# Kernel tuning notes

Hardware: AMD Instinct MI355X
Metric: run time of the kernel (lower is better)

The kernel has to match this reference:

```python
import jax, jax.numpy as jnp
import numpy as np

B, IN_DIM, N, L = 8, 2, 512, 64
D_MODEL = 32
D_FF = 32          # must equal D_MODEL: output_bn is BatchNorm2d(d_model) applied to skip
DEPTH = 3          # blocks=3 * layers=1; dilation resets to 1 each block -> all dilations = 1
KS = 2             # temporal kernel size
EPS = 1e-5         # BatchNorm eps


def setup_inputs() -> dict:
    key = jax.random.key(0)
    ks = jax.random.split(key, 16)
    s = 0.1  # weight scale for numeric sanity
    x = jax.random.normal(ks[0], (B, IN_DIM, N, L), jnp.float32)
    a = jax.random.uniform(ks[1], (N, N), jnp.float32)
    adj = a / a.sum(axis=1, keepdims=True)  # row-stochastic diffusion matrix
    return {
        "x": x,
        "adj": adj,
        "Wstart": jax.random.normal(ks[2], (D_MODEL, IN_DIM), jnp.float32) * s,
        "bstart": jnp.zeros((D_MODEL,), jnp.float32),
        "Wf": jax.random.normal(ks[3], (DEPTH, D_MODEL, D_MODEL, KS), jnp.float32) * s,
        "bf": jnp.zeros((DEPTH, D_MODEL), jnp.float32),
        "Wg": jax.random.normal(ks[4], (DEPTH, D_MODEL, D_MODEL, KS), jnp.float32) * s,
        "bg": jnp.zeros((DEPTH, D_MODEL), jnp.float32),
        "Wskip": jax.random.normal(ks[5], (DEPTH, D_FF, D_MODEL), jnp.float32) * s,
        "bskip": jnp.zeros((DEPTH, D_FF), jnp.float32),
        "Wgc": jax.random.normal(ks[6], (DEPTH, D_MODEL, 3 * D_MODEL), jnp.float32) * s,
        "bgc": jnp.zeros((DEPTH, D_MODEL), jnp.float32),
        "gcbn_g": jnp.ones((DEPTH, D_MODEL), jnp.float32),
        "gcbn_b": jnp.zeros((DEPTH, D_MODEL), jnp.float32),
        "bn_g": jnp.ones((DEPTH, D_MODEL), jnp.float32),
        "bn_b": jnp.zeros((DEPTH, D_MODEL), jnp.float32),
        "obn_g": jnp.ones((D_MODEL,), jnp.float32),
        "obn_b": jnp.zeros((D_MODEL,), jnp.float32),
    }


def _c1x1(x, W, b):
    # Conv2d with (1,1) kernel == channel mixing. x: [b,c,n,l], W: [o,c]
    return jnp.einsum('bcnl,oc->bonl', x, W) + b[None, :, None, None]


def _dconv(x, W, b, d):
    # Conv2d kernel (1,2), dilation d along time (valid). W: [o,c,2]
    Lx = x.shape[-1]
    y = (jnp.einsum('bcnl,oc->bonl', x[..., :Lx - d], W[..., 0])
         + jnp.einsum('bcnl,oc->bonl', x[..., d:], W[..., 1]))
    return y + b[None, :, None, None]


def _bn(x, g, bta):
    # eval-mode BatchNorm2d: running_mean=0, running_var=1
    inv = g / jnp.sqrt(1.0 + EPS)
    return x * inv[None, :, None, None] + bta[None, :, None, None]


def reference(x, adj, Wstart, bstart, Wf, bf, Wg, bg, Wskip, bskip,
              Wgc, bgc, gcbn_g, gcbn_b, bn_g, bn_b, obn_g, obn_b):
    rf = 1 + DEPTH * (KS - 1)  # receptive field with dilation 1 per layer
    h = _c1x1(x, Wstart, bstart)
    if h.shape[-1] < rf:
        h = jnp.pad(h, ((0, 0), (0, 0), (0, 0), (rf - h.shape[-1], 0)))
    skip = None
    for i in range(DEPTH):
        residual = h
        filt = jnp.tanh(_dconv(h, Wf[i], bf[i], 1))
        gate = jax.nn.sigmoid(_dconv(h, Wg[i], bg[i], 1))
        h = filt * gate
        s = _c1x1(h, Wskip[i], bskip[i])
        skip = s if skip is None else s + skip[..., -s.shape[-1]:]
        if i == DEPTH - 1:
            break
        # order-2 graph diffusion: h, A h, A^2 h -> concat -> 1x1 conv -> BN (dropout: eval noop)
        x1 = jnp.einsum('bcnl,nm->bcml', h, adj)
        x2 = jnp.einsum('bcnl,nm->bcml', x1, adj)
        cat = jnp.concatenate([h, x1, x2], axis=1)
        g = _bn(_c1x1(cat, Wgc[i], bgc[i]), gcbn_g[i], gcbn_b[i])
        h = g + residual[..., -g.shape[-1]:]
        h = _bn(h, bn_g[i], bn_b[i])
    out = _bn(skip, obn_g, obn_b)
    return jnp.swapaxes(out, 1, 3)  # [B, L', N, C]
```

## Files before the change

### kernel.cpp

```cpp
#include <hip/hip_runtime.h>
#include <hip/hip_bf16.h>

#define B_     8
#define CIN_   2
#define N_     512
#define C_     32
#define L_     64
#define LOUT_  61
#define BUF_   ((size_t)(8*32*512*64))

typedef __hip_bfloat16 bf16;
typedef unsigned short ushort_t;
typedef unsigned int u32;
typedef __attribute__((ext_vector_type(8))) unsigned short us8;
typedef __attribute__((ext_vector_type(8))) short bf16x8;
typedef __attribute__((ext_vector_type(4))) float f32x4;

static __device__ __forceinline__ float bits2f(ushort_t u) {
    return __uint_as_float(((unsigned)u) << 16);
}
static __device__ __forceinline__ ushort_t f2bits(float v) {
    unsigned u = __float_as_uint(v);
    return (ushort_t)((u + 0x7fffu + ((u >> 16) & 1u)) >> 16);
}

static __device__ __forceinline__ void gload16(const ushort_t* g, ushort_t* l) {
    __builtin_amdgcn_global_load_lds(
        (const __attribute__((address_space(1))) unsigned int*)g,
        (__attribute__((address_space(3))) unsigned int*)l,
        16, 0, 0);
}

static __device__ __forceinline__ u32 swap1(u32 v) {
    return (u32)__builtin_amdgcn_update_dpp(0, (int)v, 0xB1, 0xF, 0xF, true);
}

__global__ void k_start(const float* __restrict__ x,
                        const float* __restrict__ Wst,
                        const float* __restrict__ bst,
                        ushort_t* __restrict__ h) {
    int idx = blockIdx.x * 256 + threadIdx.x;
    int l0 = (idx & 7) * 8;
    int n  = (idx >> 3) & 511;
    int o  = (idx >> 12) & 31;
    int b  = idx >> 17;
    float w0 = Wst[o * 2], w1 = Wst[o * 2 + 1], bb = bst[o];
    int xbase = (b * CIN_ * N_ + n) * L_ + l0;
    float va[8], vb[8];
    *(float4*)&va[0] = *(const float4*)(x + xbase);
    *(float4*)&va[4] = *(const float4*)(x + xbase + 4);
    *(float4*)&vb[0] = *(const float4*)(x + xbase + N_ * L_);
    *(float4*)&vb[4] = *(const float4*)(x + xbase + N_ * L_ + 4);
    us8 r;
    #pragma unroll
    for (int k = 0; k < 8; ++k) r[k] = f2bits(bb + va[k] * w0 + vb[k] * w1);
    *(us8*)(h + (size_t)idx * 8) = r;
}

__global__ void k_transA(const float* __restrict__ adj, ushort_t* __restrict__ adjT) {
    __shared__ float buf[64][65];
    int ti = blockIdx.x & 7;
    int tj = blockIdx.x >> 3;
    int t = threadIdx.x;
    for (int r = 0; r < 16; ++r) {
        int e = t + 256 * r;
        int rl = e >> 6, cl = e & 63;
        buf[rl][cl] = adj[(size_t)(ti * 64 + rl) * 512 + tj * 64 + cl];
    }
    __syncthreads();
    for (int r = 0; r < 16; ++r) {
        int e = t + 256 * r;
        int ml = e >> 6, nl = e & 63;
        adjT[(size_t)(tj * 64 + ml) * 512 + ti * 64 + nl] = f2bits(buf[nl][ml]);
    }
}

__global__ __launch_bounds__(256, 2) void k_sq(const ushort_t* __restrict__ adjT,
                                               ushort_t* __restrict__ adj2T) {
    __shared__ __align__(16) ushort_t lds2[8192];
    ushort_t* As = lds2;
    ushort_t* Bs = lds2 + 4096;
    int mt = blockIdx.x & 7, nc = blockIdx.x >> 3;
    int t = threadIdx.x, lane = t & 63, w = t >> 6;
    int la = lane & 15, q = lane >> 4;
    f32x4 acc[4];
    #pragma unroll
    for (int mi = 0; mi < 4; ++mi) acc[mi] = (f32x4)0.f;
    for (int p0 = 0; p0 < 512; p0 += 64) {
        __syncthreads();
        #pragma unroll
        for (int r = 0; r < 2; ++r) {
            int e = t + 256 * r, ml = e >> 3, oct = e & 7;
            int sw = ((oct + (ml >> 3)) & 7) << 3;
            *(us8*)(As + ml * 64 + sw) =
                *(const us8*)(adjT + (size_t)(mt * 64 + ml) * 512 + p0 + oct * 8);
            *(us8*)(Bs + ml * 64 + sw) =
                *(const us8*)(adjT + (size_t)(p0 + ml) * 512 + nc * 64 + oct * 8);
        }
        __syncthreads();
        #pragma unroll
        for (int ks = 0; ks < 2; ++ks) {
            bf16x8 a[4];
            #pragma unroll
            for (int mi = 0; mi < 4; ++mi) {
                int m = mi * 16 + la;
                int bl = (ks * 4 + q + (m >> 3)) & 7;
                a[mi] = *(const bf16x8*)(As + m * 64 + bl * 8);
            }
            bf16x8 bv;
            {
                int n = w * 16 + la;
                int rot = ((n >> 3) + ks * 4 + q) & 7;
                int col = rot * 8 + (n & 7);
                const ushort_t* p = Bs + (ks * 32 + q * 8) * 64 + col;
                #pragma unroll
                for (int j = 0; j < 8; ++j) bv[j] = (short)p[j * 64];
            }
            #pragma unroll
            for (int mi = 0; mi < 4; ++mi)
                acc[mi] = __builtin_amdgcn_mfma_f32_16x16x32_bf16(a[mi], bv, acc[mi], 0, 0, 0);
        }
    }
    __syncthreads();
    ushort_t* Ys = lds2;
    #pragma unroll
    for (int mi = 0; mi < 4; ++mi)
        #pragma unroll
        for (int r = 0; r < 4; ++r)
            Ys[(mi * 16 + q * 4 + r) * 72 + w * 16 + la] = f2bits(acc[mi][r]);
    __syncthreads();
    #pragma unroll
    for (int r = 0; r < 2; ++r) {
        int e = t + 256 * r, ml = e >> 3, oct = e & 7;
        us8 v = *(const us8*)(Ys + ml * 72 + oct * 8);
        *(us8*)(adj2T + (size_t)(mt * 64 + ml) * 512 + nc * 64 + oct * 8) = v;
    }
}

__global__ __launch_bounds__(256, 4) void k_gs_mfma(
        const ushort_t* __restrict__ h,
        const float* __restrict__ Wf, const float* __restrict__ bfp,
        const float* __restrict__ Wg, const float* __restrict__ bgp,
        const float* __restrict__ Wsk, const float* __restrict__ bsk,
        ushort_t* __restrict__ G, float* __restrict__ out,
        int off, int mode, int storeG,
        const float* __restrict__ og, const float* __restrict__ obb) {
    __shared__ __align__(16) ushort_t lds[9984];
    ushort_t* Hs  = lds;
    ushort_t* Asf = lds + 4096;
    ushort_t* Asg = lds + 6400;
    ushort_t* As2 = lds + 8704;
    __shared__ float bfv[32], bgv[32], bsv[32];
    int t = threadIdx.x;
    int b = blockIdx.x >> 8, n0 = (blockIdx.x & 255) * 2;
    int lane = t & 63, w = t >> 6;
    int ng = w & 1, cg = w >> 1;
    int la = lane & 15, q = lane >> 4;

    const ushort_t* hb = h + (size_t)(b * 32) * 512 * 64;
    #pragma unroll
    for (int r = 0; r < 2; ++r) {
        int e = t + 256 * r;
        int row = e >> 3, s = e & 7;
        int og_ = ((s - row - (row >> 5)) & 7) * 8;
        gload16(hb + ((size_t)(row >> 1) * 512 + n0 + (row & 1)) * 64 + og_,
                Hs + (size_t)e * 8);
    }
    {
        int o = t >> 3, k8 = (t & 7) * 8;
        us8 vf, vg;
        #pragma unroll
        for (int i = 0; i < 8; ++i) {
            int k = k8 + i, c = k & 31, tap = k >> 5;
            vf[i] = f2bits(Wf[o * 64 + c * 2 + tap]);
            vg[i] = f2bits(Wg[o * 64 + c * 2 + tap]);
        }
        *(us8*)(Asf + o * 72 + k8) = vf;
        *(us8*)(Asg + o * 72 + k8) = vg;
        if (k8 < 32) {
            us8 vs;
            #pragma unroll
            for (int i = 0; i < 8; ++i) vs[i] = f2bits(Wsk[o * 32 + k8 + i]);
            *(us8*)(As2 + o * 40 + k8) = vs;
        }
        if (t < 32) { bfv[t] = bfp[t]; bgv[t] = bgp[t]; bsv[t] = bsk[t]; }
    }
    float4 oldv[4];
    #pragma unroll
    for (int i = 0; i < 4; ++i) oldv[i] = make_float4(0.f, 0.f, 0.f, 0.f);
    {
        int col = t >> 1, o0 = (t & 1) * 16;
        int nr = col >> 6, l = col & 63;
        if (mode != 0 && l < LOUT_) {
            const float* po = out + ((size_t)(b * LOUT_ + l) * 512 + n0 + nr) * 32 + o0;
            #pragma unroll
            for (int i = 0; i < 4; ++i) oldv[i] = *(const float4*)(po + i * 4);
        }
    }
    __syncthreads();

    bf16x8 af[2][2], ag[2][2];
    #pragma unroll
    for (int mt = 0; mt < 2; ++mt)
        #pragma unroll
        for (int ks = 0; ks < 2; ++ks) {
            af[mt][ks] = *(const bf16x8*)(Asf + (mt * 16 + la) * 72 + ks * 32 + q * 8);
            ag[mt][ks] = *(const bf16x8*)(Asg + (mt * 16 + la) * 72 + ks * 32 + q * 8);
        }
    bf16x8 a2[2];
    a2[0] = *(const bf16x8*)(As2 + la * 40 + q * 8);
    a2[1] = *(const bf16x8*)(As2 + (16 + la) * 40 + q * 8);

    f32x4 fa[2][2], ga[2][2];
    #pragma unroll
    for (int mt = 0; mt < 2; ++mt)
        #pragma unroll
        for (int cl = 0; cl < 2; ++cl) { fa[mt][cl] = (f32x4)0.f; ga[mt][cl] = (f32x4)0.f; }
    #pragma unroll
    for (int cl = 0; cl < 2; ++cl) {
        int ct = cg * 2 + cl;
        #pragma unroll
        for (int ks = 0; ks < 2; ++ks) {
            int le = ct * 16 + la + ks;
            bf16x8 bv;
            #pragma unroll
            for (int j = 0; j < 8; ++j) {
                int row = (q * 8 + j) * 2 + ng;
                int slot = ((le >> 3) + row + (row >> 5)) & 7;
                bv[j] = (le < 64) ? (short)Hs[row * 64 + (slot & 7) * 8 + (le & 7)] : (short)0;
            }
            #pragma unroll
            for (int mt = 0; mt < 2; ++mt) {
                fa[mt][cl] = __builtin_amdgcn_mfma_f32_16x16x32_bf16(af[mt][ks], bv, fa[mt][cl], 0, 0, 0);
                ga[mt][cl] = __builtin_amdgcn_mfma_f32_16x16x32_bf16(ag[mt][ks], bv, ga[mt][cl], 0, 0, 0);
            }
        }
    }
    __syncthreads();

    #pragma unroll
    for (int mt = 0; mt < 2; ++mt)
        #pragma unroll
        for (int cl = 0; cl < 2; ++cl)
            #pragma unroll
            for (int r = 0; r < 4; ++r) {
                int o = mt * 16 + q * 4 + r;
                float fv = fa[mt][cl][r] + bfv[o];
                float gv = ga[mt][cl][r] + bgv[o];
                float ef = __expf(2.f * fv);
                float act = (1.f - 2.f / (ef + 1.f)) * (1.f / (1.f + __expf(-gv)));
                int l = (cg * 2 + cl) * 16 + la;
                int row = o * 2 + ng;
                int slot = ((l >> 3) + row + (row >> 5)) & 7;
                Hs[row * 64 + slot * 8 + (l & 7)] = f2bits(act);
            }
    __syncthreads();

    if (storeG) {
        #pragma unroll
        for (int r = 0; r < 2; ++r) {
            int e = t + 256 * r;
            int row = e >> 3, s = e & 7;
            int og_ = (s - row - (row >> 5)) & 7;
            us8 v = *(const us8*)(Hs + (size_t)e * 8);
            *(us8*)(G + ((size_t)(b * 32 + (row >> 1)) * 512 + n0 + (row & 1)) * 64 + og_ * 8) = v;
        }
    }
    f32x4 sa[2][2];
    #pragma unroll
    for (int mt = 0; mt < 2; ++mt)
        #pragma unroll
        for (int cl = 0; cl < 2; ++cl) sa[mt][cl] = (f32x4)0.f;
    #pragma unroll
    for (int cl = 0; cl < 2; ++cl) {
        int le = (cg * 2 + cl) * 16 + la + off;
        bf16x8 bv;
        #pragma unroll
        for (int j = 0; j < 8; ++j) {
            int row = (q * 8 + j) * 2 + ng;
            int slot = ((le >> 3) + row + (row >> 5)) & 7;
            bv[j] = (le < 64) ? (short)Hs[row * 64 + (slot & 7) * 8 + (le & 7)] : (short)0;
        }
        sa[0][cl] = __builtin_amdgcn_mfma_f32_16x16x32_bf16(a2[0], bv, sa[0][cl], 0, 0, 0);
        sa[1][cl] = __builtin_amdgcn_mfma_f32_16x16x32_bf16(a2[1], bv, sa[1][cl], 0, 0, 0);
    }
    __syncthreads();

    float* St = (float*)lds;
    const float rbn = rsqrtf(1.f + 1e-5f);
    #pragma unroll
    for (int mt = 0; mt < 2; ++mt)
        #pragma unroll
        for (int cl = 0; cl < 2; ++cl) {
            int col = ng * 64 + (cg * 2 + cl) * 16 + la;
            int ob = mt * 16 + q * 4;
            float4 sv = make_float4(sa[mt][cl][0] + bsv[ob],
                                    sa[mt][cl][1] + bsv[ob + 1],
                                    sa[mt][cl][2] + bsv[ob + 2],
                                    sa[mt][cl][3] + bsv[ob + 3]);
            *(float4*)(St + col * 36 + ob) = sv;
        }
    __syncthreads();
    {
        int col = t >> 1, o0 = (t & 1) * 16;
        int nr = col >> 6, l = col & 63;
        if (l < LOUT_) {
            float* po = out + ((size_t)(b * LOUT_ + l) * 512 + n0 + nr) * 32 + o0;
            #pragma unroll
            for (int i = 0; i < 4; ++i) {
                float4 s = *(float4*)(St + col * 36 + o0 + i * 4);
                if (mode == 0) {
                    *(float4*)(po + i * 4) = s;
                } else {
                    float4 vv = make_float4(oldv[i].x + s.x, oldv[i].y + s.y,
                                            oldv[i].z + s.z, oldv[i].w + s.w);
                    if (mode == 2) {
                        int ob = o0 + i * 4;
                        vv.x = vv.x * (og[ob] * rbn) + obb[ob];
                        vv.y = vv.y * (og[ob + 1] * rbn) + obb[ob + 1];
                        vv.z = vv.z * (og[ob + 2] * rbn) + obb[ob + 2];
                        vv.w = vv.w * (og[ob + 3] * rbn) + obb[ob + 3];
                    }
                    *(float4*)(po + i * 4) = vv;
                }
            }
        }
    }
}

__global__ __launch_bounds__(256, 2) void k_diffuse2(
        const ushort_t* __restrict__ X, const ushort_t* __restrict__ adjT,
        const ushort_t* __restrict__ adj2T,
        ushort_t* __restrict__ Y1, ushort_t* __restrict__ Y2) {
    __shared__ __align__(16) ushort_t lds[32768];
    int cp = blockIdx.x & 15;
    int mt = (blockIdx.x >> 4) & 7;
    int b  = blockIdx.x >> 7;
    int t  = threadIdx.x;
    int lane = t & 63, w = t >> 6;
    int c_loc = w & 1, lh = w >> 1;
    int m0 = mt * 64;
    int la = lane & 15, q = lane >> 4;
    int p_ = la & 1;
    u32 sel = p_ ? 0x07060302u : 0x05040100u;
    const ushort_t* Xb = X + (size_t)(b * 32 + cp * 2) * 512 * 64;
    f32x4 acc1[4][2], acc2[4][2];
    #pragma unroll
    for (int mi = 0; mi < 4; ++mi)
        #pragma unroll
        for (int li = 0; li < 2; ++li) { acc1[mi][li] = (f32x4)0.f; acc2[mi][li] = (f32x4)0.f; }

    union U { u32 u[4]; bf16x8 v; };

    auto STAGE = [&](int n0, ushort_t* bb) {
        ushort_t* As1b = bb;
        ushort_t* As2b = bb + 4096;
        ushort_t* Xsb  = bb + 8192;
        #pragma unroll
        for (int r = 0; r < 2; ++r) {
            int e = t + 256 * r, ml = e >> 3, s = e & 7;
            int og = ((s - (ml >> 3)) & 7) * 8;
            gload16(adjT  + (size_t)(m0 + ml) * 512 + n0 + og, As1b + (size_t)e * 8);
            gload16(adj2T + (size_t)(m0 + ml) * 512 + n0 + og, As2b + (size_t)e * 8);
        }
        #pragma unroll
        for (int r = 0; r < 4; ++r) {
            int e = t + 256 * r;
            int cl = e >> 9, nl = (e >> 3) & 63, s = e & 7;
            int og = ((s - nl - (nl >> 3)) & 7) * 8;
            gload16(Xb + ((size_t)cl * 512 + n0 + nl) * 64 + og, Xsb + (size_t)e * 8);
        }
    };

    STAGE(0, lds);
    __syncthreads();

    for (int it = 0; it < 8; ++it) {
        ushort_t* cur = lds + (it & 1) * 16384;
        if (it < 7) STAGE((it + 1) * 64, lds + ((it + 1) & 1) * 16384);
        ushort_t* As1 = cur;
        ushort_t* As2 = cur + 4096;
        ushort_t* Xs  = cur + 8192;
        const ushort_t* xc = Xs + c_loc * 4096;
        #pragma unroll
        for (int ks = 0; ks < 2; ++ks) {
            bf16x8 a1[4], a2v[4];
            #pragma unroll
            for (int mi = 0; mi < 4; ++mi) {
                int m = mi * 16 + la;
                int bl = (ks * 4 + q + (m >> 3)) & 7;
                a1[mi]  = *(const bf16x8*)(As1 + m * 64 + bl * 8);
                a2v[mi] = *(const bf16x8*)(As2 + m * 64 + bl * 8);
            }
            bf16x8 bb[2];
            #pragma unroll
            for (int li = 0; li < 2; ++li) {
                int l2 = lh * 32 + li * 16 + (la & ~1);
                int r0 = ks * 32 + q * 8 + p_ * 4;
                int brot = ((l2 >> 3) + p_ * 4 + ks * 4 + q) & 7;
                u32 o0 = *(const u32*)(xc + (r0 + 0) * 64 + (((brot + 0) & 7) << 3) + (l2 & 7));
                u32 o1 = *(const u32*)(xc + (r0 + 1) * 64 + (((brot + 1) & 7) << 3) + (l2 & 7));
                u32 o2 = *(const u32*)(xc + (r0 + 2) * 64 + (((brot + 2) & 7) << 3) + (l2 & 7));
                u32 o3 = *(const u32*)(xc + (r0 + 3) * 64 + (((brot + 3) & 7) << 3) + (l2 & 7));
                u32 s0 = swap1(o0), s1 = swap1(o1), s2 = swap1(o2), s3 = swap1(o3);
                u32 lo0 = p_ ? s0 : o0, lo1 = p_ ? s1 : o1;
                u32 lo2 = p_ ? s2 : o2, lo3 = p_ ? s3 : o3;
                u32 hi0 = p_ ? o0 : s0, hi1 = p_ ? o1 : s1;
                u32 hi2 = p_ ? o2 : s2, hi3 = p_ ? o3 : s3;
                U u;
                u.u[0] = __builtin_amdgcn_perm(lo1, lo0, sel);
                u.u[1] = __builtin_amdgcn_perm(lo3, lo2, sel);
                u.u[2] = __builtin_amdgcn_perm(hi1, hi0, sel);
                u.u[3] = __builtin_amdgcn_perm(hi3, hi2, sel);
                bb[li] = u.v;
            }
            #pragma unroll
            for (int mi = 0; mi < 4; ++mi)
                #pragma unroll
                for (int li = 0; li < 2; ++li) {
                    acc1[mi][li] = __builtin_amdgcn_mfma_f32_16x16x32_bf16(a1[mi],  bb[li], acc1[mi][li], 0, 0, 0);
                    acc2[mi][li] = __builtin_amdgcn_mfma_f32_16x16x32_bf16(a2v[mi], bb[li], acc2[mi][li], 0, 0, 0);
                }
        }
        __syncthreads();
    }

    ushort_t* Ys = lds;
    #pragma unroll
    for (int pass = 0; pass < 2; ++pass) {
        __syncthreads();
        f32x4 (*src)[2] = pass ? acc2 : acc1;
        #pragma unroll
        for (int mi = 0; mi < 4; ++mi)
            #pragma unroll
            for (int li = 0; li < 2; ++li)
                #pragma unroll
                for (int r = 0; r < 4; ++r) {
                    int row = mi * 16 + q * 4 + r;
                    int col = lh * 32 + li * 16 + la;
                    Ys[c_loc * 4608 + row * 72 + col] = f2bits(src[mi][li][r]);
                }
        __syncthreads();
        ushort_t* Yo = pass ? Y2 : Y1;
        int c = t >> 7, mrem = t & 127;
        int m = mrem >> 1, lq = mrem & 1;
        #pragma unroll
        for (int r = 0; r < 4; ++r) {
            int l0 = lq * 32 + r * 8;
            us8 v = *(const us8*)(Ys + c * 4608 + m * 72 + l0);
            *(us8*)(Yo + ((size_t)(b * 32 + cp * 2 + c) * 512 + m0 + m) * 64 + l0) = v;
        }
    }
}

__global__ __launch_bounds__(256, 4) void k_gc3_mfma(
        ushort_t* __restrict__ G, const ushort_t* __restrict__ X1,
        const ushort_t* __restrict__ X2, const ushort_t* __restrict__ hres,
        const float* __restrict__ Wgc, const float* __restrict__ bgc,
        const float* __restrict__ gg, const float* __restrict__ gb,
        const float* __restrict__ bg2, const float* __restrict__ bb2) {
    __shared__ __align__(16) ushort_t cat[192 * 64];
    __shared__ __align__(16) ushort_t hr[64 * 64];
    __shared__ __align__(16) ushort_t Aw[32 * 104];
    __shared__ float prm[5][32];
    int t = threadIdx.x;
    int b = blockIdx.x >> 8, n0 = (blockIdx.x & 255) * 2;
    int lane = t & 63, w = t >> 6;
    int ng = w & 1, cg = w >> 1;
    int la = lane & 15, q = lane >> 4;
    int p_ = la & 1;
    u32 sel = p_ ? 0x07060302u : 0x05040100u;

    #pragma unroll
    for (int r = 0; r < 6; ++r) {
        int e = t + 256 * r;
        int row = e >> 3, s = e & 7;
        int k = row >> 1, nr = row & 1;
        int rot = k + (k >> 3);
        int og = ((s - rot) & 7) * 8;
        const ushort_t* src = (k < 32) ? G : ((k < 64) ? X1 : X2);
        gload16(src + ((size_t)(b * 32 + (k & 31)) * 512 + n0 + nr) * 64 + og,
                cat + (size_t)e * 8);
    }
    #pragma unroll
    for (int r = 0; r < 2; ++r) {
        int e = t + 256 * r;
        int row = e >> 3, oct = e & 7;
        gload16(hres + ((size_t)(b * 32 + (row >> 1)) * 512 + n0 + (row & 1)) * 64 + oct * 8,
                hr + (size_t)e * 8);
    }
    for (int e = t; e < 384; e += 256) {
        int o = e / 12, oct = e % 12;
        us8 v;
        #pragma unroll
        for (int i = 0; i < 8; ++i) v[i] = f2bits(Wgc[o * 96 + oct * 8 + i]);
        *(us8*)(Aw + o * 104 + oct * 8) = v;
    }
    if (t < 32) {
        prm[0][t] = bgc[t]; prm[1][t] = gg[t]; prm[2][t] = gb[t];
        prm[3][t] = bg2[t]; prm[4][t] = bb2[t];
    }
    __syncthreads();

    bf16x8 a[2][3];
    #pragma unroll
    for (int mt = 0; mt < 2; ++mt)
        #pragma unroll
        for (int ks = 0; ks < 3; ++ks)
            a[mt][ks] = *(const bf16x8*)(Aw + (mt * 16 + la) * 104 + ks * 32 + q * 8);

    union U { u32 u[4]; bf16x8 v; };
    f32x4 acc[2][2];
    #pragma unroll
    for (int mt = 0; mt < 2; ++mt)
        #pragma unroll
        for (int cl = 0; cl < 2; ++cl) acc[mt][cl] = (f32x4)0.f;
    #pragma unroll
    for (int cl = 0; cl < 2; ++cl) {
        int l2 = (cg * 2 + cl) * 16 + (la & ~1);
        #pragma unroll
        for (int ks = 0; ks < 3; ++ks) {
            int rb = (ks * 64 + q * 16 + p_ * 8 + ng);
            int brot = ((l2 >> 3) + p_ * 4 + ks * 4 + q) & 7;
            u32 o0 = *(const u32*)(cat + (rb + 0) * 64 + (((brot + 0) & 7) << 3) + (l2 & 7));
            u32 o1 = *(const u32*)(cat + (rb + 2) * 64 + (((brot + 1) & 7) << 3) + (l2 & 7));
            u32 o2 = *(const u32*)(cat + (rb + 4) * 64 + (((brot + 2) & 7) << 3) + (l2 & 7));
            u32 o3 = *(const u32*)(cat + (rb + 6) * 64 + (((brot + 3) & 7) << 3) + (l2 & 7));
            u32 s0 = swap1(o0), s1 = swap1(o1), s2 = swap1(o2), s3 = swap1(o3);
            u32 lo0 = p_ ? s0 : o0, lo1 = p_ ? s1 : o1;
            u32 lo2 = p_ ? s2 : o2, lo3 = p_ ? s3 : o3;
            u32 hi0 = p_ ? o0 : s0, hi1 = p_ ? o1 : s1;
            u32 hi2 = p_ ? o2 : s2, hi3 = p_ ? o3 : s3;
            U u;
            u.u[0] = __builtin_amdgcn_perm(lo1, lo0, sel);
            u.u[1] = __builtin_amdgcn_perm(lo3, lo2, sel);
            u.u[2] = __builtin_amdgcn_perm(hi1, hi0, sel);
            u.u[3] = __builtin_amdgcn_perm(hi3, hi2, sel);
            acc[0][cl] = __builtin_amdgcn_mfma_f32_16x16x32_bf16(a[0][ks], u.v, acc[0][cl], 0, 0, 0);
            acc[1][cl] = __builtin_amdgcn_mfma_f32_16x16x32_bf16(a[1][ks], u.v, acc[1][cl], 0, 0, 0);
        }
    }
    __syncthreads();

    const float rbn = rsqrtf(1.f + 1e-5f);
    #pragma unroll
    for (int mt = 0; mt < 2; ++mt)
        #pragma unroll
        for (int cl = 0; cl < 2; ++cl)
            #pragma unroll
            for (int r = 0; r < 4; ++r) {
                int o = mt * 16 + q * 4 + r;
                int l = (cg * 2 + cl) * 16 + la;
                float v = acc[mt][cl][r] + prm[0][o];
                v = v * (prm[1][o] * rbn) + prm[2][o];
                float res = (l < 63) ? bits2f(hr[(o * 2 + ng) * 64 + l + 1]) : 0.f;
                v = (v + res) * (prm[3][o] * rbn) + prm[4][o];
                int row = o * 2 + ng;
                int rot = o + (o >> 3);
                int slot = ((l >> 3) + rot) & 7;
                cat[row * 64 + slot * 8 + (l & 7)] = f2bits(v);
            }
    __syncthreads();
    #pragma unroll
    for (int r = 0; r < 2; ++r) {
        int e = t + 256 * r;
        int row = e >> 3, og = e & 7;
        int o = row >> 1, nr = row & 1;
        int slot = (og + o + (o >> 3)) & 7;
        us8 v = *(const us8*)(cat + row * 64 + slot * 8);
        *(us8*)(G + ((size_t)(b * 32 + o) * 512 + n0 + nr) * 64 + og * 8) = v;
    }
}

extern "C" void kernel_launch(void* const* d_in, const int* in_sizes, int n_in,
                              void* d_out, int out_size, void* d_ws, size_t ws_size,
                              hipStream_t stream) {
    const float* x      = (const float*)d_in[0];
    const float* adj    = (const float*)d_in[1];
    const float* Wstart = (const float*)d_in[2];
    const float* bstart = (const float*)d_in[3];
    const float* Wf     = (const float*)d_in[4];
    const float* bf_    = (const float*)d_in[5];
    const float* Wg     = (const float*)d_in[6];
    const float* bg     = (const float*)d_in[7];
    const float* Wskip  = (const float*)d_in[8];
    const float* bskip  = (const float*)d_in[9];
    const float* Wgc    = (const float*)d_in[10];
    const float* bgc    = (const float*)d_in[11];
    const float* gcbn_g = (const float*)d_in[12];
    const float* gcbn_b = (const float*)d_in[13];
    const float* bn_g   = (const float*)d_in[14];
    const float* bn_b   = (const float*)d_in[15];
    const float* obn_g  = (const float*)d_in[16];
    const float* obn_b  = (const float*)d_in[17];
    float* out = (float*)d_out;

    ushort_t* P0    = (ushort_t*)d_ws;
    ushort_t* P1    = P0 + BUF_;
    ushort_t* P2    = P1 + BUF_;
    ushort_t* P3    = P2 + BUF_;
    ushort_t* adjT  = P3 + BUF_;
    ushort_t* adj2T = adjT + 512 * 512;

    k_transA<<<64, 256, 0, stream>>>(adj, adjT);
    k_sq<<<64, 256, 0, stream>>>(adjT, adj2T);
    k_start<<<4096, 256, 0, stream>>>(x, Wstart, bstart, P0);

    ushort_t* h  = P0;
    ushort_t* Gb = P1;
    for (int i = 0; i < 3; ++i) {
        int mode = (i == 0) ? 0 : ((i == 2) ? 2 : 1);
        k_gs_mfma<<<2048, 256, 0, stream>>>(h, Wf + i * 2048, bf_ + i * 32,
                                            Wg + i * 2048, bg + i * 32,
                                            Wskip + i * 1024, bskip + i * 32,
                                            Gb, out, 2 - i, mode, (i < 2) ? 1 : 0,
                                            obn_g, obn_b);
        if (i == 2) break;
        k_diffuse2<<<1024, 256, 0, stream>>>(Gb, adjT, adj2T, P2, P3);
        k_gc3_mfma<<<2048, 256, 0, stream>>>(Gb, P2, P3, h,
                                             Wgc + i * 3072, bgc + i * 32,
                                             gcbn_g + i * 32, gcbn_b + i * 32,
                                             bn_g + i * 32, bn_b + i * 32);
        ushort_t* tmp = h; h = Gb; Gb = tmp;
    }
}
```

Before: 303.4 us.

## Retile diffusion kernel to one channel per block, load adjacency directly from global

The diffusion kernel now handles one channel per block instead of two, doubling the grid and halving LDS so four blocks fit per CU. Adjacency A and A^2 fragments are read straight from global memory into registers rather than staged through shared memory; only the X tile is double-buffered in LDS. The aim is higher occupancy and less LDS traffic. The cost is that each block re-reads the adjacency tiles from global/L2 with half the reuse per load, which adds cache pressure.

```diff
diff --git a/kernel.cpp b/kernel.cpp
--- a/kernel.cpp
+++ b/kernel.cpp
@@ -328,47 +328,34 @@
     }
 }
 
-__global__ __launch_bounds__(256, 2) void k_diffuse2(
+__global__ __launch_bounds__(256, 4) void k_diffuse2(
         const ushort_t* __restrict__ X, const ushort_t* __restrict__ adjT,
         const ushort_t* __restrict__ adj2T,
         ushort_t* __restrict__ Y1, ushort_t* __restrict__ Y2) {
-    __shared__ __align__(16) ushort_t lds[32768];
-    int cp = blockIdx.x & 15;
-    int mt = (blockIdx.x >> 4) & 7;
-    int b  = blockIdx.x >> 7;
+    __shared__ __align__(16) ushort_t lds[16384];
+    int c  = blockIdx.x & 31;
+    int mt = (blockIdx.x >> 5) & 7;
+    int b  = blockIdx.x >> 8;
     int t  = threadIdx.x;
     int lane = t & 63, w = t >> 6;
-    int c_loc = w & 1, lh = w >> 1;
     int m0 = mt * 64;
     int la = lane & 15, q = lane >> 4;
     int p_ = la & 1;
     u32 sel = p_ ? 0x07060302u : 0x05040100u;
-    const ushort_t* Xb = X + (size_t)(b * 32 + cp * 2) * 512 * 64;
-    f32x4 acc1[4][2], acc2[4][2];
-    #pragma unroll
-    for (int mi = 0; mi < 4; ++mi)
-        #pragma unroll
-        for (int li = 0; li < 2; ++li) { acc1[mi][li] = (f32x4)0.f; acc2[mi][li] = (f32x4)0.f; }
+    const ushort_t* Xb = X + (size_t)(b * 32 + c) * 512 * 64;
+    f32x4 acc1[4], acc2[4];
+    #pragma unroll
+    for (int mi = 0; mi < 4; ++mi) { acc1[mi] = (f32x4)0.f; acc2[mi] = (f32x4)0.f; }
 
     union U { u32 u[4]; bf16x8 v; };
 
-    auto STAGE = [&](int n0, ushort_t* bb) {
-        ushort_t* As1b = bb;
-        ushort_t* As2b = bb + 4096;
-        ushort_t* Xsb  = bb + 8192;
+    auto STAGE = [&](int n0, ushort_t* Xsb) {
         #pragma unroll
         for (int r = 0; r < 2; ++r) {
-            int e = t + 256 * r, ml = e >> 3, s = e & 7;
-            int og = ((s - (ml >> 3)) & 7) * 8;
-            gload16(adjT  + (size_t)(m0 + ml) * 512 + n0 + og, As1b + (size_t)e * 8);
-            gload16(adj2T + (size_t)(m0 + ml) * 512 + n0 + og, As2b + (size_t)e * 8);
-        }
-        #pragma unroll
-        for (int r = 0; r < 4; ++r) {
             int e = t + 256 * r;
-            int cl = e >> 9, nl = (e >> 3) & 63, s = e & 7;
+            int nl = e >> 3, s = e & 7;
             int og = ((s - nl - (nl >> 3)) & 7) * 8;
-            gload16(Xb + ((size_t)cl * 512 + n0 + nl) * 64 + og, Xsb + (size_t)e * 8);
+            gload16(Xb + ((size_t)(n0 + nl)) * 64 + og, Xsb + (size_t)e * 8);
         }
     };
 
@@ -376,51 +363,40 @@
     __syncthreads();
 
     for (int it = 0; it < 8; ++it) {
-        ushort_t* cur = lds + (it & 1) * 16384;
-        if (it < 7) STAGE((it + 1) * 64, lds + ((it + 1) & 1) * 16384);
-        ushort_t* As1 = cur;
-        ushort_t* As2 = cur + 4096;
-        ushort_t* Xs  = cur + 8192;
-        const ushort_t* xc = Xs + c_loc * 4096;
+        ushort_t* Xs = lds + (it & 1) * 8192;
+        if (it < 7) STAGE((it + 1) * 64, lds + ((it + 1) & 1) * 8192);
+        int n0 = it * 64;
         #pragma unroll
         for (int ks = 0; ks < 2; ++ks) {
             bf16x8 a1[4], a2v[4];
             #pragma unroll
             for (int mi = 0; mi < 4; ++mi) {
-                int m = mi * 16 + la;
-                int bl = (ks * 4 + q + (m >> 3)) & 7;
-                a1[mi]  = *(const bf16x8*)(As1 + m * 64 + bl * 8);
-                a2v[mi] = *(const bf16x8*)(As2 + m * 64 + bl * 8);
-            }
-            bf16x8 bb[2];
-            #pragma unroll
-            for (int li = 0; li < 2; ++li) {
-                int l2 = lh * 32 + li * 16 + (la & ~1);
-                int r0 = ks * 32 + q * 8 + p_ * 4;
-                int brot = ((l2 >> 3) + p_ * 4 + ks * 4 + q) & 7;
-                u32 o0 = *(const u32*)(xc + (r0 + 0) * 64 + (((brot + 0) & 7) << 3) + (l2 & 7));
-                u32 o1 = *(const u32*)(xc + (r0 + 1) * 64 + (((brot + 1) & 7) << 3) + (l2 & 7));
-                u32 o2 = *(const u32*)(xc + (r0 + 2) * 64 + (((brot + 2) & 7) << 3) + (l2 & 7));
-                u32 o3 = *(const u32*)(xc + (r0 + 3) * 64 + (((brot + 3) & 7) << 3) + (l2 & 7));
-                u32 s0 = swap1(o0), s1 = swap1(o1), s2 = swap1(o2), s3 = swap1(o3);
-                u32 lo0 = p_ ? s0 : o0, lo1 = p_ ? s1 : o1;
-                u32 lo2 = p_ ? s2 : o2, lo3 = p_ ? s3 : o3;
-                u32 hi0 = p_ ? o0 : s0, hi1 = p_ ? o1 : s1;
-                u32 hi2 = p_ ? o2 : s2, hi3 = p_ ? o3 : s3;
-                U u;
-                u.u[0] = __builtin_amdgcn_perm(lo1, lo0, sel);
-                u.u[1] = __builtin_amdgcn_perm(lo3, lo2, sel);
-                u.u[2] = __builtin_amdgcn_perm(hi1, hi0, sel);
-                u.u[3] = __builtin_amdgcn_perm(hi3, hi2, sel);
-                bb[li] = u.v;
-            }
-            #pragma unroll
-            for (int mi = 0; mi < 4; ++mi)
-                #pragma unroll
-                for (int li = 0; li < 2; ++li) {
-                    acc1[mi][li] = __builtin_amdgcn_mfma_f32_16x16x32_bf16(a1[mi],  bb[li], acc1[mi][li], 0, 0, 0);
-                    acc2[mi][li] = __builtin_amdgcn_mfma_f32_16x16x32_bf16(a2v[mi], bb[li], acc2[mi][li], 0, 0, 0);
-                }
+                size_t ao = (size_t)(m0 + mi * 16 + la) * 512 + n0 + ks * 32 + q * 8;
+                a1[mi]  = *(const bf16x8*)(adjT  + ao);
+                a2v[mi] = *(const bf16x8*)(adj2T + ao);
+            }
+            int l2 = w * 16 + (la & ~1);
+            int r0 = ks * 32 + q * 8 + p_ * 4;
+            int brot = ((l2 >> 3) + p_ * 4 + ks * 4 + q) & 7;
+            u32 o0 = *(const u32*)(Xs + (r0 + 0) * 64 + (((brot + 0) & 7) << 3) + (l2 & 7));
+            u32 o1 = *(const u32*)(Xs + (r0 + 1) * 64 + (((brot + 1) & 7) << 3) + (l2 & 7));
+            u32 o2 = *(const u32*)(Xs + (r0 + 2) * 64 + (((brot + 2) & 7) << 3) + (l2 & 7));
+            u32 o3 = *(const u32*)(Xs + (r0 + 3) * 64 + (((brot + 3) & 7) << 3) + (l2 & 7));
+            u32 s0 = swap1(o0), s1 = swap1(o1), s2 = swap1(o2), s3 = swap1(o3);
+            u32 lo0 = p_ ? s0 : o0, lo1 = p_ ? s1 : o1;
+            u32 lo2 = p_ ? s2 : o2, lo3 = p_ ? s3 : o3;
+            u32 hi0 = p_ ? o0 : s0, hi1 = p_ ? o1 : s1;
+            u32 hi2 = p_ ? o2 : s2, hi3 = p_ ? o3 : s3;
+            U u;
+            u.u[0] = __builtin_amdgcn_perm(lo1, lo0, sel);
+            u.u[1] = __builtin_amdgcn_perm(lo3, lo2, sel);
+            u.u[2] = __builtin_amdgcn_perm(hi1, hi0, sel);
+            u.u[3] = __builtin_amdgcn_perm(hi3, hi2, sel);
+            #pragma unroll
+            for (int mi = 0; mi < 4; ++mi) {
+                acc1[mi] = __builtin_amdgcn_mfma_f32_16x16x32_bf16(a1[mi],  u.v, acc1[mi], 0, 0, 0);
+                acc2[mi] = __builtin_amdgcn_mfma_f32_16x16x32_bf16(a2v[mi], u.v, acc2[mi], 0, 0, 0);
+            }
         }
         __syncthreads();
     }
@@ -429,26 +405,20 @@
     #pragma unroll
     for (int pass = 0; pass < 2; ++pass) {
         __syncthreads();
-        f32x4 (*src)[2] = pass ? acc2 : acc1;
+        f32x4* src = pass ? acc2 : acc1;
         #pragma unroll
         for (int mi = 0; mi < 4; ++mi)
             #pragma unroll
-            for (int li = 0; li < 2; ++li)
-                #pragma unroll
-                for (int r = 0; r < 4; ++r) {
-                    int row = mi * 16 + q * 4 + r;
-                    int col = lh * 32 + li * 16 + la;
-                    Ys[c_loc * 4608 + row * 72 + col] = f2bits(src[mi][li][r]);
-                }
+            for (int r = 0; r < 4; ++r)
+                Ys[(mi * 16 + q * 4 + r) * 72 + w * 16 + la] = f2bits(src[mi][r]);
         __syncthreads();
         ushort_t* Yo = pass ? Y2 : Y1;
-        int c = t >> 7, mrem = t & 127;
-        int m = mrem >> 1, lq = mrem & 1;
-        #pragma unroll
-        for (int r = 0; r < 4; ++r) {
-            int l0 = lq * 32 + r * 8;
-            us8 v = *(const us8*)(Ys + c * 4608 + m * 72 + l0);
-            *(us8*)(Yo + ((size_t)(b * 32 + cp * 2 + c) * 512 + m0 + m) * 64 + l0) = v;
+        #pragma unroll
+        for (int r = 0; r < 2; ++r) {
+            int e = t + 256 * r;
+            int m = e >> 3, oct = e & 7;
+            us8 v = *(const us8*)(Ys + m * 72 + oct * 8);
+            *(us8*)(Yo + ((size_t)(b * 32 + c) * 512 + m0 + m) * 64 + oct * 8) = v;
         }
     }
 }
@@ -616,7 +586,7 @@
                                             Gb, out, 2 - i, mode, (i < 2) ? 1 : 0,
                                             obn_g, obn_b);
         if (i == 2) break;
-        k_diffuse2<<<1024, 256, 0, stream>>>(Gb, adjT, adj2T, P2, P3);
+        k_diffuse2<<<2048, 256, 0, stream>>>(Gb, adjT, adj2T, P2, P3);
         k_gc3_mfma<<<2048, 256, 0, stream>>>(Gb, P2, P3, h,
                                              Wgc + i * 3072, bgc + i * 32,
                                              gcbn_g + i * 32, gcbn_b + i * 32,
```

After: 469.4 us. +54.7%, slower.
